# Optimization experiments

Measured on AMD Instinct MI355X. Metric: run time of the kernel, lower is better.

The kernel has to match this reference:

```python
import jax, jax.numpy as jnp
import numpy as np

B, L, D, H = 4, 1024, 768, 12
DH = D // H  # 64


def setup_inputs() -> dict:
    key = jax.random.key(0)
    kx, kk, kq, kv = jax.random.split(key, 4)
    # Original uses torch.rand (uniform [0,1)); scale by 1/D so pre-softmax
    # logits stay in a numerically sane range (same math, better conditioning).
    scale = 1.0 / D
    x = jax.random.normal(kx, (B, L, D), dtype=jnp.float32)
    k = jax.random.uniform(kk, (H, D, D), dtype=jnp.float32) * scale
    q = jax.random.uniform(kq, (H, D, D), dtype=jnp.float32) * scale
    v = jax.random.uniform(kv, (H, DH, D), dtype=jnp.float32) * scale
    return {"x": x, "k": k, "q": q, "v": v}


def reference(x, k, q, v):
    # x: [B, L, D]; torch permutes to [B, D, L] then 'bdl,ncd->bncl';
    # equivalent directly: 'bld,ncd->bncl'.
    K = jnp.einsum('bld,ncd->bncl', x, k)   # [B, H, D, L]
    Q = jnp.einsum('bld,ncd->bncl', x, q)   # [B, H, D, L]
    V = jnp.einsum('bld,ncd->bncl', x, v)   # [B, H, DH, L]
    scores = jnp.einsum('bndl,bndm->bnlm', Q, K)        # [B, H, L, L]
    S = jax.nn.softmax(scores, axis=-1)                  # softmax over dim 3
    R = jnp.einsum('bnkl,bndl->bndk', S, V)              # [B, H, DH, L]
    R = R.reshape(x.shape[0], D, -1)                     # [B, D, L]
    return jnp.transpose(R, (0, 2, 1))                   # [B, L, D]
```

## Files before the change

kernel.cpp:

```cpp
#include <hip/hip_runtime.h>
#include <hip/hip_bf16.h>
#include <stdint.h>
#include <stddef.h>

typedef unsigned short u16;
typedef __attribute__((ext_vector_type(8))) short short8;
typedef __attribute__((ext_vector_type(4))) float f32x4;
typedef __attribute__((ext_vector_type(16))) float f32x16;

#define NB 4
#define NL 1024
#define ND 768
#define NH 12
#define NDH 64

__device__ __forceinline__ u16 f2bf(float f) {
  __hip_bfloat16 h = __float2bfloat16(f);
  return *reinterpret_cast<u16*>(&h);
}
__device__ __forceinline__ float bf2f(u16 u) {
  __hip_bfloat16 h;
  *reinterpret_cast<u16*>(&h) = u;
  return __bfloat162float(h);
}

__device__ __forceinline__ void load16_to_lds(const u16* g, u16* l) {
  __builtin_amdgcn_global_load_lds(
      (__attribute__((address_space(1))) void*)(uintptr_t)g,
      (__attribute__((address_space(3))) void*)(uint32_t)(uintptr_t)l,
      16, 0, 0);
}

__global__ __launch_bounds__(256) void cast_bf16_kernel(const float* __restrict__ in,
                                                        u16* __restrict__ out, int n4) {
  int i = blockIdx.x * 256 + threadIdx.x;
  int stride = gridDim.x * 256;
  for (; i < n4; i += stride) {
    float4 f = ((const float4*)in)[i];
    ushort4 o;
    o.x = f2bf(f.x); o.y = f2bf(f.y); o.z = f2bf(f.z); o.w = f2bf(f.w);
    ((ushort4*)out)[i] = o;
  }
}

__global__ __launch_bounds__(256) void transpose_cast2_kernel(const float* __restrict__ qI,
                                                              const float* __restrict__ kI,
                                                              u16* __restrict__ qT,
                                                              u16* __restrict__ kTp) {
  __shared__ float tile[32][33];
  int hz = blockIdx.z;
  int h = (hz < NH) ? hz : hz - NH;
  const float* src = ((hz < NH) ? qI : kI) + (size_t)h * ND * ND;
  u16* dst = ((hz < NH) ? qT : kTp) + (size_t)h * ND * ND;
  int c0 = blockIdx.x * 32, r0 = blockIdx.y * 32;
  int tx = threadIdx.x & 31, ty = threadIdx.x >> 5;
#pragma unroll
  for (int i = 0; i < 32; i += 8)
    tile[ty + i][tx] = src[(size_t)(r0 + ty + i) * ND + c0 + tx];
  __syncthreads();
#pragma unroll
  for (int i = 0; i < 32; i += 8)
    dst[(size_t)(c0 + ty + i) * ND + r0 + tx] = f2bf(tile[tx][ty + i]);
}

template <bool BF16_OUT, int IM, int IN, int KDIM, int LDC>
__global__ __launch_bounds__(256, 4) void gemm_bt(
    const u16* __restrict__ A, const u16* __restrict__ Bm, void* __restrict__ Cv,
    long sAb, long sAn, long sAz,
    long sBb, long sBn, long sBz,
    long sCb, long sCn, long sCz,
    int p0) {
  constexpr int BK = 64;
  constexpr int MTILE = IM * 64;
  constexpr int NTILE = IN * 64;
  constexpr int CPR = BK / 8;
  constexpr int ACH = MTILE * CPR / 256;
  constexpr int BCH = NTILE * CPR / 256;
  __shared__ __align__(16) u16 As[MTILE * BK];
  __shared__ __align__(16) u16 Bs[NTILE * BK];

  int id = blockIdx.x + gridDim.x * (blockIdx.y + gridDim.y * blockIdx.z);
  int total = gridDim.x * gridDim.y * gridDim.z;
  int xx, yy, zz;
  if ((total & 7) == 0) {
    int per = total >> 3;
    int wk = (id & 7) * per + (id >> 3);
    xx = wk % gridDim.x;
    int g2 = wk / gridDim.x;
    yy = g2 % gridDim.y;
    zz = g2 / gridDim.y;
  } else {
    xx = blockIdx.x; yy = blockIdx.y; zz = blockIdx.z;
  }

  int g = p0 + zz;
  int b = g / NH, n = g % NH;
  A  += (size_t)b * sAb + (size_t)n * sAn + (size_t)zz * sAz;
  Bm += (size_t)b * sBb + (size_t)n * sBn + (size_t)zz * sBz;
  size_t cOff = (size_t)b * sCb + (size_t)n * sCn + (size_t)zz * sCz;

  int m0 = yy * MTILE, n0 = xx * NTILE;
  int t = threadIdx.x;
  int lane = t & 63, w = t >> 6;
  int m32 = lane & 31, kg = lane >> 5;
  int wm = w >> 1, wn = w & 1;

  const u16* gAb;
  const u16* gBb;
  {
    int r = t / CPR;
    int cc = (t & (CPR - 1)) ^ (r & 7);
    gAb = A + (size_t)(m0 + r) * KDIM + cc * 8;
    gBb = Bm + (size_t)(n0 + r) * KDIM + cc * 8;
  }

  f32x16 acc[IM][IN];
#pragma unroll
  for (int i = 0; i < IM; i++)
#pragma unroll
    for (int j = 0; j < IN; j++)
#pragma unroll
      for (int r = 0; r < 16; r++) acc[i][j][r] = 0.f;

#pragma unroll 1
  for (int k0 = 0; k0 < KDIM; k0 += BK) {
    __syncthreads();
#pragma unroll
    for (int u = 0; u < ACH; u++)
      load16_to_lds(gAb + (size_t)u * 32 * KDIM, &As[(size_t)(u * 256 + w * 64) * 8]);
    gAb += BK;
#pragma unroll
    for (int u = 0; u < BCH; u++)
      load16_to_lds(gBb + (size_t)u * 32 * KDIM, &Bs[(size_t)(u * 256 + w * 64) * 8]);
    gBb += BK;
    __syncthreads();

#pragma unroll
    for (int kc = 0; kc < 2; kc++) {
      short8 af[IM][2], bfr[IN][2];
#pragma unroll
      for (int i = 0; i < IM; i++) {
        int row = wm * (IM * 32) + i * 32 + m32;
#pragma unroll
        for (int h = 0; h < 2; h++) {
          int ck = (kc * 4 + h * 2 + kg) ^ (row & 7);
          af[i][h] = *(const short8*)&As[row * BK + ck * 8];
        }
      }
#pragma unroll
      for (int j = 0; j < IN; j++) {
        int row = wn * (IN * 32) + j * 32 + m32;
#pragma unroll
        for (int h = 0; h < 2; h++) {
          int ck = (kc * 4 + h * 2 + kg) ^ (row & 7);
          bfr[j][h] = *(const short8*)&Bs[row * BK + ck * 8];
        }
      }
#pragma unroll
      for (int i = 0; i < IM; i++)
#pragma unroll
        for (int j = 0; j < IN; j++) {
          acc[i][j] = __builtin_amdgcn_mfma_f32_32x32x16_bf16(af[i][0], bfr[j][0], acc[i][j], 0, 0, 0);
          acc[i][j] = __builtin_amdgcn_mfma_f32_32x32x16_bf16(af[i][1], bfr[j][1], acc[i][j], 0, 0, 0);
        }
    }
  }

#pragma unroll
  for (int i = 0; i < IM; i++) {
#pragma unroll
    for (int j = 0; j < IN; j++) {
      int colg = n0 + wn * (IN * 32) + j * 32 + m32;
#pragma unroll
      for (int r = 0; r < 16; r++) {
        int rowg = m0 + wm * (IM * 32) + i * 32 + (r & 3) + 8 * (r >> 2) + 4 * kg;
        float vv = acc[i][j][r];
        if (BF16_OUT) {
          ((u16*)Cv)[cOff + (size_t)rowg * LDC + colg] = f2bf(vv);
        } else {
          ((float*)Cv)[cOff + (size_t)rowg * LDC + colg] = vv;
        }
      }
    }
  }
}

template <bool BF16_OUT, int KDIM, int LDC>
__global__ __launch_bounds__(512, 2) void gemm256_bt(
    const u16* __restrict__ A, const u16* __restrict__ Bm, void* __restrict__ Cv,
    long sAb, long sAn, long sAz,
    long sBb, long sBn, long sBz,
    long sCb, long sCn, long sCz,
    int p0) {
  constexpr int BK = 64;
  constexpr int NT = KDIM / BK;
  static_assert(KDIM % BK == 0 && NT >= 3, "pipeline needs >=3 K-tiles");
  __shared__ __align__(16) u16 As[2][256 * BK];
  __shared__ __align__(16) u16 Bs[2][256 * BK];

  int id = blockIdx.x + gridDim.x * (blockIdx.y + gridDim.y * blockIdx.z);
  int total = gridDim.x * gridDim.y * gridDim.z;
  int xx, yy, zz;
  if ((total & 7) == 0) {
    int per = total >> 3;
    int wk = (id & 7) * per + (id >> 3);
    xx = wk % gridDim.x;
    int g2 = wk / gridDim.x;
    yy = g2 % gridDim.y;
    zz = g2 / gridDim.y;
  } else {
    xx = blockIdx.x; yy = blockIdx.y; zz = blockIdx.z;
  }

  int g = p0 + zz;
  int b = g / NH, n = g % NH;
  A  += (size_t)b * sAb + (size_t)n * sAn + (size_t)zz * sAz;
  Bm += (size_t)b * sBb + (size_t)n * sBn + (size_t)zz * sBz;
  size_t cOff = (size_t)b * sCb + (size_t)n * sCn + (size_t)zz * sCz;

  int m0 = yy * 256, n0 = xx * 256;
  int t = threadIdx.x;
  int lane = t & 63, w = t >> 6;
  int wm = w >> 2, wn = w & 3;
  int l15 = lane & 15, q4 = lane >> 4;

  int r0 = t >> 3;
  int cc0 = (t & 7) ^ (r0 & 7);
  const u16* gA = A + (size_t)(m0 + r0) * KDIM + cc0 * 8;
  const u16* gB = Bm + (size_t)(n0 + r0) * KDIM + cc0 * 8;

  u16* Ac = &As[0][0]; u16* Ao = &As[1][0];
  u16* Bc = &Bs[0][0]; u16* Bo = &Bs[1][0];
  int ldsOff = w * 64 * 8;

#define STG_A(dst, k0, u) load16_to_lds(gA + (size_t)(u) * 64 * KDIM + (k0), (dst) + (u) * 512 * 8 + ldsOff)
#define STG_B(dst, k0, u) load16_to_lds(gB + (size_t)(u) * 64 * KDIM + (k0), (dst) + (u) * 512 * 8 + ldsOff)

#define READ_A(buf, H, dst) do { \
  _Pragma("unroll") for (int fm = 0; fm < 4; fm++) { \
    int row = (H) * 128 + wm * 64 + fm * 16 + l15; \
    _Pragma("unroll") for (int ks = 0; ks < 2; ks++) { \
      int ck = (ks * 4 + q4) ^ (row & 7); \
      dst[fm][ks] = *(const short8*)((buf) + row * 64 + ck * 8); \
    } \
  } \
} while (0)

#define READ_B(buf, G, dst) do { \
  _Pragma("unroll") for (int fn = 0; fn < 2; fn++) { \
    int row = (G) * 128 + wn * 32 + fn * 16 + l15; \
    _Pragma("unroll") for (int ks = 0; ks < 2; ks++) { \
      int ck = (ks * 4 + q4) ^ (row & 7); \
      dst[fn][ks] = *(const short8*)((buf) + row * 64 + ck * 8); \
    } \
  } \
} while (0)

#define MFMA_PH(H, G, AR, BR) do { \
  __builtin_amdgcn_s_setprio(1); \
  _Pragma("unroll") for (int ks = 0; ks < 2; ks++) \
    _Pragma("unroll") for (int fm = 0; fm < 4; fm++) \
      _Pragma("unroll") for (int fn = 0; fn < 2; fn++) \
        acc[H][G][fm][fn] = __builtin_amdgcn_mfma_f32_16x16x32_bf16(AR[fm][ks], BR[fn][ks], acc[H][G][fm][fn], 0, 0, 0); \
  __builtin_amdgcn_s_setprio(0); \
} while (0)

  f32x4 acc[2][2][4][2];
#pragma unroll
  for (int h = 0; h < 2; h++)
#pragma unroll
    for (int gg = 0; gg < 2; gg++)
#pragma unroll
      for (int fm = 0; fm < 4; fm++)
#pragma unroll
        for (int fn = 0; fn < 2; fn++)
          acc[h][gg][fm][fn] = (f32x4){0.f, 0.f, 0.f, 0.f};

  STG_A(Ac, 0, 0); STG_A(Ac, 0, 1); STG_A(Ac, 0, 2); STG_A(Ac, 0, 3);
  STG_B(Bc, 0, 0); STG_B(Bc, 0, 1); STG_B(Bc, 0, 2); STG_B(Bc, 0, 3);
  STG_A(Ao, BK, 0); STG_A(Ao, BK, 1);
  asm volatile("s_waitcnt vmcnt(2)" ::: "memory");
  __builtin_amdgcn_s_barrier();
  __builtin_amdgcn_sched_barrier(0);

#pragma unroll 1
  for (int tk = 0; tk < NT; ++tk) {
    short8 af[4][2], bf0[2][2], bf1[2][2];
    if (tk + 1 < NT) {
      int kn1 = (tk + 1) * BK;
      STG_A(Ao, kn1, 2); STG_A(Ao, kn1, 3);
      STG_B(Bo, kn1, 0); STG_B(Bo, kn1, 1); STG_B(Bo, kn1, 2); STG_B(Bo, kn1, 3);
    }
    READ_A(Ac, 0, af);
    READ_B(Bc, 0, bf0);
    MFMA_PH(0, 0, af, bf0);
    READ_B(Bc, 1, bf1);
    MFMA_PH(0, 1, af, bf1);
    __builtin_amdgcn_sched_barrier(0);
    asm volatile("s_waitcnt lgkmcnt(0)" ::: "memory");
    __builtin_amdgcn_s_barrier();
    __builtin_amdgcn_sched_barrier(0);
    if (tk + 2 < NT) {
      int kn2 = (tk + 2) * BK;
      STG_A(Ac, kn2, 0); STG_A(Ac, kn2, 1);
    }
    READ_A(Ac, 1, af);
    MFMA_PH(1, 0, af, bf0);
    MFMA_PH(1, 1, af, bf1);
    if (tk + 1 < NT) {
      __builtin_amdgcn_sched_barrier(0);
      asm volatile("s_waitcnt lgkmcnt(0)" ::: "memory");
      if (tk + 2 < NT) {
        asm volatile("s_waitcnt vmcnt(2)" ::: "memory");
      } else {
        asm volatile("s_waitcnt vmcnt(0)" ::: "memory");
      }
      __builtin_amdgcn_s_barrier();
      __builtin_amdgcn_sched_barrier(0);
    }
    u16* tp = Ac; Ac = Ao; Ao = tp;
    tp = Bc; Bc = Bo; Bo = tp;
  }

#pragma unroll
  for (int h = 0; h < 2; h++)
#pragma unroll
    for (int gg = 0; gg < 2; gg++)
#pragma unroll
      for (int fm = 0; fm < 4; fm++)
#pragma unroll
        for (int fn = 0; fn < 2; fn++) {
          int colg = n0 + gg * 128 + wn * 32 + fn * 16 + l15;
#pragma unroll
          for (int r = 0; r < 4; r++) {
            int rowg = m0 + h * 128 + wm * 64 + fm * 16 + q4 * 4 + r;
            float vv = acc[h][gg][fm][fn][r];
            if (BF16_OUT) {
              ((u16*)Cv)[cOff + (size_t)rowg * LDC + colg] = f2bf(vv);
            } else {
              ((float*)Cv)[cOff + (size_t)rowg * LDC + colg] = vv;
            }
          }
        }
#undef STG_A
#undef STG_B
#undef READ_A
#undef READ_B
#undef MFMA_PH
}

__global__ __launch_bounds__(256) void softmax_pv_kernel(
    const u16* __restrict__ Sb, const u16* __restrict__ V2, float* __restrict__ out,
    int p0) {
  __shared__ __align__(16) u16 Ps[64 * 128];
  __shared__ __align__(16) u16 Vs[64 * 128];

  int id = blockIdx.x + gridDim.x * blockIdx.y;
  int total = gridDim.x * gridDim.y;
  int xx, zz;
  if ((total & 7) == 0) {
    int per = total >> 3;
    int wk = (id & 7) * per + (id >> 3);
    xx = wk & 15; zz = wk >> 4;
  } else {
    xx = blockIdx.x; zz = blockIdx.y;
  }

  int g = p0 + zz;
  int b = g / NH, n = g % NH;
  const u16* S = Sb + (size_t)zz * NL * NL;
  const u16* V = V2 + (size_t)g * NDH * NL;

  int l0 = xx * 64;
  int t = threadIdx.x;
  int lane = t & 63, w = t >> 6;
  int row16 = lane & 15, q = lane >> 4;
  int rs = row16 & 7;

  f32x4 acc[5];
#pragma unroll
  for (int j = 0; j < 5; j++) acc[j] = (f32x4){0.f, 0.f, 0.f, 0.f};

  short8 onesf;
  {
    short val = (row16 == 0) ? (short)0x3F80 : (short)0;
#pragma unroll
    for (int e = 0; e < 8; e++) onesf[e] = val;
  }

  const u16* ssrc[4];
  const u16* vsrc[4];
#pragma unroll
  for (int u = 0; u < 4; u++) {
    int c = u * 256 + t;
    int r = c >> 4, cc = (c & 15) ^ (r & 7);
    ssrc[u] = S + (size_t)(l0 + r) * NL + cc * 8;
    vsrc[u] = V + (size_t)r * NL + cc * 8;
  }

#pragma unroll 1
  for (int mt = 0; mt < 8; mt++) {
    int mo = mt * 128;
    __syncthreads();
#pragma unroll
    for (int u = 0; u < 4; u++)
      load16_to_lds(ssrc[u] + mo, &Ps[(size_t)(u * 256 + w * 64) * 8]);
#pragma unroll
    for (int u = 0; u < 4; u++)
      load16_to_lds(vsrc[u] + mo, &Vs[(size_t)(u * 256 + w * 64) * 8]);
    __syncthreads();

#pragma unroll
    for (int kk = 0; kk < 4; kk++) {
      int ch = ((kk * 4 + q) ^ rs) * 16;
      int lrow = w * 16 + row16;
      short8 raw = *(const short8*)((const char*)Ps + lrow * 256 + ch);
      short8 af;
#pragma unroll
      for (int e = 0; e < 8; e++) af[e] = (short)f2bf(__expf(bf2f((u16)raw[e])));
      short8 bfr[4];
#pragma unroll
      for (int j = 0; j < 4; j++) {
        int dh = j * 16 + row16;
        bfr[j] = *(const short8*)((const char*)Vs + dh * 256 + ch);
      }
#pragma unroll
      for (int j = 0; j < 4; j++)
        acc[j] = __builtin_amdgcn_mfma_f32_16x16x32_bf16(af, bfr[j], acc[j], 0, 0, 0);
      acc[4] = __builtin_amdgcn_mfma_f32_16x16x32_bf16(af, onesf, acc[4], 0, 0, 0);
    }
  }

#pragma unroll
  for (int r = 0; r < 4; r++) {
    float sum = __shfl(acc[4][r], lane & 48, 64);
    float inv = 1.0f / sum;
    int row = l0 + w * 16 + q * 4 + r;
    float* op = out + ((size_t)b * NL + row) * ND + n * NDH;
#pragma unroll
    for (int j = 0; j < 4; j++)
      op[j * 16 + row16] = acc[j][r] * inv;
  }
}

extern "C" void kernel_launch(void* const* d_in, const int* in_sizes, int n_in,
                              void* d_out, int out_size, void* d_ws, size_t ws_size,
                              hipStream_t stream) {
  (void)in_sizes; (void)n_in; (void)out_size;
  const float* x  = (const float*)d_in[0];
  const float* kI = (const float*)d_in[1];
  const float* qI = (const float*)d_in[2];
  const float* vI = (const float*)d_in[3];
  float* out = (float*)d_out;

  size_t off = 0;
  char* wsb = (char*)d_ws;
  auto alloc = [&](size_t bytes) -> char* {
    char* p = wsb + off;
    off += (bytes + 255) & ~(size_t)255;
    return p;
  };
  u16* xb = (u16*)alloc((size_t)NB * NL * ND * 2);
  u16* qT = (u16*)alloc((size_t)NH * ND * ND * 2);
  u16* kT = (u16*)alloc((size_t)NH * ND * ND * 2);
  u16* vb = (u16*)alloc((size_t)NH * NDH * ND * 2);
  u16* MT = (u16*)alloc((size_t)NH * ND * ND * 2);
  u16* V2 = (u16*)alloc((size_t)NB * NH * NDH * NL * 2);
  size_t fixedSz = off;
  const size_t perPair = (size_t)NL * ND * 2 + (size_t)NL * NL * 2;
  int chunk = NB * NH;
  if (fixedSz + (size_t)chunk * perPair > ws_size) {
    size_t avail = ws_size > fixedSz ? ws_size - fixedSz : 0;
    chunk = (int)(avail / perPair);
    if (chunk < 1) chunk = 1;
    if (chunk > NB * NH) chunk = NB * NH;
  }
  u16* T  = (u16*)alloc((size_t)chunk * NL * ND * 2);
  u16* Sb = (u16*)alloc((size_t)chunk * NL * NL * 2);

  const long DD  = (long)ND * ND;
  const long LD  = (long)NL * ND;
  const long LL  = (long)NL * NL;
  const long DHL = (long)NDH * NL;

  {
    int n4 = NB * NL * ND / 4;
    cast_bf16_kernel<<<dim3((n4 + 255) / 256), dim3(256), 0, stream>>>(x, xb, n4);
    int n4v = NH * NDH * ND / 4;
    cast_bf16_kernel<<<dim3((n4v + 255) / 256), dim3(256), 0, stream>>>(vI, vb, n4v);
  }
  transpose_cast2_kernel<<<dim3(24, 24, 2 * NH), dim3(256), 0, stream>>>(qI, kI, qT, kT);

  gemm_bt<true, 2, 2, 768, ND><<<dim3(6, 6, NH), dim3(256), 0, stream>>>(
      kT, qT, MT,
      0, DD, 0,  0, DD, 0,  0, DD, 0, 0);

  gemm_bt<true, 2, 2, 768, NL><<<dim3(8, 6, NB), dim3(256), 0, stream>>>(
      vb, xb, V2,
      0, 0, 0,  0, 0, LD,  0, 0, (long)NH * DHL, 0);

  for (int p0 = 0; p0 < NB * NH; p0 += chunk) {
    int c = NB * NH - p0;
    if (c > chunk) c = chunk;
    gemm256_bt<true, 768, ND><<<dim3(3, 4, c), dim3(512), 0, stream>>>(
        xb, MT, T,
        LD, 0, 0,  0, DD, 0,  0, 0, LD, p0);
    gemm256_bt<true, 768, NL><<<dim3(4, 4, c), dim3(512), 0, stream>>>(
        T, xb, Sb,
        0, 0, LD,  LD, 0, 0,  0, 0, LL, p0);
    softmax_pv_kernel<<<dim3(16, c), dim3(256), 0, stream>>>(Sb, V2, out, p0);
  }
}
```

Baseline: 315.7 us.

## Restructure 256x256 GEMM into an eight-phase ping-pong pipeline with per-quadrant staging

Replaces the two-phase-per-K-tile main loop of the 256-tile bf16 GEMM with an eight-phase schedule over two K-tiles per iteration. Each quadrant of the output tile gets its own barrier-delimited MFMA phase, and global-to-LDS loads for the next tiles are issued in half-slabs between phases. The goal is to interleave LDS reads, global loads and MFMA work more finely so matrix-core stalls are hidden. In exchange there are many more barriers per iteration, and KDIM must now be a multiple of 128.

```diff
diff --git a/kernel.cpp b/kernel.cpp
--- a/kernel.cpp
+++ b/kernel.cpp
@@ -186,7 +186,7 @@
 }
 
 template <bool BF16_OUT, int KDIM, int LDC>
-__global__ __launch_bounds__(512, 2) void gemm256_bt(
+__global__ __launch_bounds__(512, 2) void gemm256_8p(
     const u16* __restrict__ A, const u16* __restrict__ Bm, void* __restrict__ Cv,
     long sAb, long sAn, long sAz,
     long sBb, long sBn, long sBz,
@@ -194,7 +194,8 @@
     int p0) {
   constexpr int BK = 64;
   constexpr int NT = KDIM / BK;
-  static_assert(KDIM % BK == 0 && NT >= 3, "pipeline needs >=3 K-tiles");
+  constexpr int NC = NT / 2;
+  static_assert(KDIM % 128 == 0 && NC >= 2, "need even #K-tiles and >=2 cycles");
   __shared__ __align__(16) u16 As[2][256 * BK];
   __shared__ __align__(16) u16 Bs[2][256 * BK];
 
@@ -228,113 +229,133 @@
   int cc0 = (t & 7) ^ (r0 & 7);
   const u16* gA = A + (size_t)(m0 + r0) * KDIM + cc0 * 8;
   const u16* gB = Bm + (size_t)(n0 + r0) * KDIM + cc0 * 8;
-
-  u16* Ac = &As[0][0]; u16* Ao = &As[1][0];
-  u16* Bc = &Bs[0][0]; u16* Bo = &Bs[1][0];
-  int ldsOff = w * 64 * 8;
-
-#define STG_A(dst, k0, u) load16_to_lds(gA + (size_t)(u) * 64 * KDIM + (k0), (dst) + (u) * 512 * 8 + ldsOff)
-#define STG_B(dst, k0, u) load16_to_lds(gB + (size_t)(u) * 64 * KDIM + (k0), (dst) + (u) * 512 * 8 + ldsOff)
-
-#define READ_A(buf, H, dst) do { \
+  int wslab = w * 512;
+
+#define STG_A1(d, h, u, kt) load16_to_lds( \
+    gA + (size_t)((h) * 128 + (u) * 64) * KDIM + (size_t)(kt) * BK, \
+    &As[d][((h) * 128 + (u) * 64) * BK + wslab])
+#define STG_B1(d, h, u, kt) load16_to_lds( \
+    gB + (size_t)((h) * 128 + (u) * 64) * KDIM + (size_t)(kt) * BK, \
+    &Bs[d][((h) * 128 + (u) * 64) * BK + wslab])
+#define STG_A2(d, h, kt) do { STG_A1(d, h, 0, kt); STG_A1(d, h, 1, kt); } while (0)
+#define STG_B2(d, h, kt) do { STG_B1(d, h, 0, kt); STG_B1(d, h, 1, kt); } while (0)
+
+#define READ_A(d, qm, dst) do { \
   _Pragma("unroll") for (int fm = 0; fm < 4; fm++) { \
-    int row = (H) * 128 + wm * 64 + fm * 16 + l15; \
+    int row = (qm) * 128 + wm * 64 + fm * 16 + l15; \
     _Pragma("unroll") for (int ks = 0; ks < 2; ks++) { \
       int ck = (ks * 4 + q4) ^ (row & 7); \
-      dst[fm][ks] = *(const short8*)((buf) + row * 64 + ck * 8); \
+      dst[fm][ks] = *(const short8*)&As[d][row * BK + ck * 8]; \
     } \
   } \
 } while (0)
 
-#define READ_B(buf, G, dst) do { \
+#define READ_B(d, qn, dst) do { \
   _Pragma("unroll") for (int fn = 0; fn < 2; fn++) { \
-    int row = (G) * 128 + wn * 32 + fn * 16 + l15; \
+    int row = (qn) * 128 + wn * 32 + fn * 16 + l15; \
     _Pragma("unroll") for (int ks = 0; ks < 2; ks++) { \
       int ck = (ks * 4 + q4) ^ (row & 7); \
-      dst[fn][ks] = *(const short8*)((buf) + row * 64 + ck * 8); \
+      dst[fn][ks] = *(const short8*)&Bs[d][row * BK + ck * 8]; \
     } \
   } \
 } while (0)
 
-#define MFMA_PH(H, G, AR, BR) do { \
+#define MF_Q(qm, qn, AR, BR) do { \
   __builtin_amdgcn_s_setprio(1); \
   _Pragma("unroll") for (int ks = 0; ks < 2; ks++) \
     _Pragma("unroll") for (int fm = 0; fm < 4; fm++) \
       _Pragma("unroll") for (int fn = 0; fn < 2; fn++) \
-        acc[H][G][fm][fn] = __builtin_amdgcn_mfma_f32_16x16x32_bf16(AR[fm][ks], BR[fn][ks], acc[H][G][fm][fn], 0, 0, 0); \
+        acc[qm][qn][fm][fn] = __builtin_amdgcn_mfma_f32_16x16x32_bf16( \
+            AR[fm][ks], BR[fn][ks], acc[qm][qn][fm][fn], 0, 0, 0); \
   __builtin_amdgcn_s_setprio(0); \
 } while (0)
 
+#define PH_SYNC() do { \
+  __builtin_amdgcn_s_barrier(); \
+  asm volatile("s_waitcnt lgkmcnt(0)" ::: "memory"); \
+  __builtin_amdgcn_sched_barrier(0); \
+} while (0)
+#define PH_END() do { \
+  __builtin_amdgcn_s_barrier(); \
+  __builtin_amdgcn_sched_barrier(0); \
+} while (0)
+
   f32x4 acc[2][2][4][2];
 #pragma unroll
-  for (int h = 0; h < 2; h++)
-#pragma unroll
-    for (int gg = 0; gg < 2; gg++)
+  for (int qm = 0; qm < 2; qm++)
+#pragma unroll
+    for (int qn = 0; qn < 2; qn++)
 #pragma unroll
       for (int fm = 0; fm < 4; fm++)
 #pragma unroll
         for (int fn = 0; fn < 2; fn++)
-          acc[h][gg][fm][fn] = (f32x4){0.f, 0.f, 0.f, 0.f};
-
-  STG_A(Ac, 0, 0); STG_A(Ac, 0, 1); STG_A(Ac, 0, 2); STG_A(Ac, 0, 3);
-  STG_B(Bc, 0, 0); STG_B(Bc, 0, 1); STG_B(Bc, 0, 2); STG_B(Bc, 0, 3);
-  STG_A(Ao, BK, 0); STG_A(Ao, BK, 1);
-  asm volatile("s_waitcnt vmcnt(2)" ::: "memory");
+          acc[qm][qn][fm][fn] = (f32x4){0.f, 0.f, 0.f, 0.f};
+
+  STG_A2(0, 0, 0); STG_A2(0, 1, 0);
+  STG_B2(0, 0, 0); STG_B2(0, 1, 0);
+  STG_A2(1, 0, 1); STG_B2(1, 0, 1);
+  asm volatile("s_waitcnt vmcnt(4)" ::: "memory");
   __builtin_amdgcn_s_barrier();
   __builtin_amdgcn_sched_barrier(0);
 
 #pragma unroll 1
-  for (int tk = 0; tk < NT; ++tk) {
-    short8 af[4][2], bf0[2][2], bf1[2][2];
-    if (tk + 1 < NT) {
-      int kn1 = (tk + 1) * BK;
-      STG_A(Ao, kn1, 2); STG_A(Ao, kn1, 3);
-      STG_B(Bo, kn1, 0); STG_B(Bo, kn1, 1); STG_B(Bo, kn1, 2); STG_B(Bo, kn1, 3);
+  for (int cyc = 0; cyc < NC; ++cyc) {
+    int t0 = cyc * 2;
+    bool full = (cyc + 1 < NC);
+    short8 af0[4][2], af1[4][2], bq0[2][2], bq1[2][2];
+
+    READ_A(0, 0, af0); READ_B(0, 0, bq0);
+    STG_A2(1, 1, t0 + 1);
+    PH_SYNC(); MF_Q(0, 0, af0, bq0); PH_END();
+    READ_B(0, 1, bq1);
+    STG_B2(1, 1, t0 + 1);
+    PH_SYNC(); MF_Q(0, 1, af0, bq1); PH_END();
+    READ_A(0, 1, af1);
+    if (full) STG_A2(0, 0, t0 + 2);
+    PH_SYNC(); MF_Q(1, 0, af1, bq0); PH_END();
+    if (full) STG_B2(0, 0, t0 + 2);
+    __builtin_amdgcn_s_barrier();
+    MF_Q(1, 1, af1, bq1);
+    __builtin_amdgcn_sched_barrier(0);
+    if (full) asm volatile("s_waitcnt vmcnt(4)" ::: "memory");
+    else      asm volatile("s_waitcnt vmcnt(0)" ::: "memory");
+    PH_END();
+
+    READ_A(1, 0, af0); READ_B(1, 0, bq0);
+    if (full) STG_A2(0, 1, t0 + 2);
+    PH_SYNC(); MF_Q(0, 0, af0, bq0); PH_END();
+    READ_B(1, 1, bq1);
+    if (full) STG_B2(0, 1, t0 + 2);
+    PH_SYNC(); MF_Q(0, 1, af0, bq1); PH_END();
+    READ_A(1, 1, af1);
+    if (full) STG_A2(1, 0, t0 + 3);
+    PH_SYNC(); MF_Q(1, 0, af1, bq0); PH_END();
+    if (full) {
+      STG_B2(1, 0, t0 + 3);
+      __builtin_amdgcn_s_barrier();
+      MF_Q(1, 1, af1, bq1);
+      __builtin_amdgcn_sched_barrier(0);
+      asm volatile("s_waitcnt vmcnt(4)" ::: "memory");
+      PH_END();
+    } else {
+      __builtin_amdgcn_s_barrier();
+      MF_Q(1, 1, af1, bq1);
     }
-    READ_A(Ac, 0, af);
-    READ_B(Bc, 0, bf0);
-    MFMA_PH(0, 0, af, bf0);
-    READ_B(Bc, 1, bf1);
-    MFMA_PH(0, 1, af, bf1);
-    __builtin_amdgcn_sched_barrier(0);
-    asm volatile("s_waitcnt lgkmcnt(0)" ::: "memory");
-    __builtin_amdgcn_s_barrier();
-    __builtin_amdgcn_sched_barrier(0);
-    if (tk + 2 < NT) {
-      int kn2 = (tk + 2) * BK;
-      STG_A(Ac, kn2, 0); STG_A(Ac, kn2, 1);
-    }
-    READ_A(Ac, 1, af);
-    MFMA_PH(1, 0, af, bf0);
-    MFMA_PH(1, 1, af, bf1);
-    if (tk + 1 < NT) {
-      __builtin_amdgcn_sched_barrier(0);
-      asm volatile("s_waitcnt lgkmcnt(0)" ::: "memory");
-      if (tk + 2 < NT) {
-        asm volatile("s_waitcnt vmcnt(2)" ::: "memory");
-      } else {
-        asm volatile("s_waitcnt vmcnt(0)" ::: "memory");
-      }
-      __builtin_amdgcn_s_barrier();
-      __builtin_amdgcn_sched_barrier(0);
-    }
-    u16* tp = Ac; Ac = Ao; Ao = tp;
-    tp = Bc; Bc = Bo; Bo = tp;
-  }
-
-#pragma unroll
-  for (int h = 0; h < 2; h++)
-#pragma unroll
-    for (int gg = 0; gg < 2; gg++)
+  }
+
+#pragma unroll
+  for (int qm = 0; qm < 2; qm++)
+#pragma unroll
+    for (int qn = 0; qn < 2; qn++)
 #pragma unroll
       for (int fm = 0; fm < 4; fm++)
 #pragma unroll
         for (int fn = 0; fn < 2; fn++) {
-          int colg = n0 + gg * 128 + wn * 32 + fn * 16 + l15;
+          int colg = n0 + qn * 128 + wn * 32 + fn * 16 + l15;
 #pragma unroll
           for (int r = 0; r < 4; r++) {
-            int rowg = m0 + h * 128 + wm * 64 + fm * 16 + q4 * 4 + r;
-            float vv = acc[h][gg][fm][fn][r];
+            int rowg = m0 + qm * 128 + wm * 64 + fm * 16 + q4 * 4 + r;
+            float vv = acc[qm][qn][fm][fn][r];
             if (BF16_OUT) {
               ((u16*)Cv)[cOff + (size_t)rowg * LDC + colg] = f2bf(vv);
             } else {
@@ -342,11 +363,15 @@
             }
           }
         }
-#undef STG_A
-#undef STG_B
+#undef STG_A1
+#undef STG_B1
+#undef STG_A2
+#undef STG_B2
 #undef READ_A
 #undef READ_B
-#undef MFMA_PH
+#undef MF_Q
+#undef PH_SYNC
+#undef PH_END
 }
 
 __global__ __launch_bounds__(256) void softmax_pv_kernel(
@@ -502,10 +527,10 @@
   for (int p0 = 0; p0 < NB * NH; p0 += chunk) {
     int c = NB * NH - p0;
     if (c > chunk) c = chunk;
-    gemm256_bt<true, 768, ND><<<dim3(3, 4, c), dim3(512), 0, stream>>>(
+    gemm256_8p<true, 768, ND><<<dim3(3, 4, c), dim3(512), 0, stream>>>(
         xb, MT, T,
         LD, 0, 0,  0, DD, 0,  0, 0, LD, p0);
-    gemm256_bt<true, 768, NL><<<dim3(4, 4, c), dim3(512), 0, stream>>>(
+    gemm256_8p<true, 768, NL><<<dim3(4, 4, c), dim3(512), 0, stream>>>(
         T, xb, Sb,
         0, 0, LD,  LD, 0, 0,  0, 0, LL, p0);
     softmax_pv_kernel<<<dim3(16, c), dim3(256), 0, stream>>>(Sb, V2, out, p0);
```

After: 326.2 us. +3.3%, slower.
